# Optimization experiments

Measured on AMD Instinct MI355X. Metric: run time of the kernel, lower is better.

## Reference

```python
import jax, jax.numpy as jnp
import numpy as np

N_NODES = 100000
N_EDGES = 1250000
IN_DIM, HID_DIM, OUT_DIM = 128, 64, 64
NUM_LAYERS = 3
EPS = 1e-12  # F.normalize eps


def setup_inputs() -> dict:
    key = jax.random.key(0)
    ks = jax.random.split(key, 10)
    s = 0.05
    x = jax.random.normal(ks[0], (N_NODES, IN_DIM), dtype=jnp.float32)
    edge_index = jax.random.randint(ks[1], (2, N_EDGES), 0, N_NODES, dtype=jnp.int32)
    W1 = jax.random.normal(ks[2], (IN_DIM, HID_DIM), dtype=jnp.float32) * s
    b1 = jax.random.normal(ks[3], (HID_DIM,), dtype=jnp.float32) * s
    Wl = jax.random.normal(ks[4], (NUM_LAYERS, HID_DIM, HID_DIM), dtype=jnp.float32) * s
    bl = jax.random.normal(ks[5], (NUM_LAYERS, HID_DIM), dtype=jnp.float32) * s
    Wr = jax.random.normal(ks[6], (NUM_LAYERS, HID_DIM, HID_DIM), dtype=jnp.float32) * s
    W2 = jax.random.normal(ks[7], (HID_DIM, OUT_DIM), dtype=jnp.float32) * s
    b2 = jax.random.normal(ks[8], (OUT_DIM,), dtype=jnp.float32) * s
    return {"x": x, "edge_index": edge_index, "W1": W1, "b1": b1,
            "Wl": Wl, "bl": bl, "Wr": Wr, "W2": W2, "b2": b2}


def reference(x, edge_index, W1, b1, Wl, bl, Wr, W2, b2):
    n = x.shape[0]
    src, dst = edge_index[0], edge_index[1]
    # in-degree for mean aggregation (zero-degree -> aggregate stays 0)
    deg = jax.ops.segment_sum(jnp.ones_like(dst, dtype=x.dtype), dst, num_segments=n)
    inv_deg = jnp.where(deg > 0, 1.0 / jnp.maximum(deg, 1.0), 0.0)[:, None]  # [n,1]
    h = x @ W1 + b1  # [n, hid]
    for i in range(Wl.shape[0]):
        # gather source features, scatter-mean to destinations
        agg = jax.ops.segment_sum(h[src], dst, num_segments=n) * inv_deg  # [n, hid]
        o = agg @ Wl[i] + bl[i] + h @ Wr[i]
        # row-wise L2 normalize (PyG normalize=True)
        norm = jnp.sqrt(jnp.sum(o * o, axis=-1, keepdims=True))
        o = o / jnp.maximum(norm, EPS)
        h = jax.nn.relu(o)
    return h @ W2 + b2
```

## Files before the change

### kernel.cpp

```cpp
#include <hip/hip_runtime.h>
#include <hip/hip_bf16.h>


#define NT 256
#define BATCH 4096
#define SBCAP 8192
#define HSTRIDE 72

typedef __attribute__((ext_vector_type(8))) short bf16x8;
typedef __attribute__((ext_vector_type(4))) float f32x4;

__device__ __forceinline__ float bfbits2f(unsigned short b) {
    return __uint_as_float(((unsigned)b) << 16);
}
__device__ __forceinline__ unsigned short f2bfbits(float v) {
    __hip_bfloat16 b = __float2bfloat16(v);
    return *reinterpret_cast<unsigned short*>(&b);
}


__global__ __launch_bounds__(NT) void bin1_kernel(const int* __restrict__ src,
    const int* __restrict__ dst, int m, unsigned* __restrict__ gcur,
    unsigned* __restrict__ bins) {
    __shared__ unsigned hist[256];
    __shared__ unsigned gbase[256];
    const int t = threadIdx.x;
    const int base = blockIdx.x * BATCH;
    hist[t] = 0;
    __syncthreads();
    int d[16], s[16];
    const int e0 = base + t * 16;
    const bool full = (base + BATCH) <= m;
    if (full) {
        #pragma unroll
        for (int q = 0; q < 4; ++q) {
            const int4 dv = *(const int4*)&dst[e0 + q * 4];
            const int4 sv = *(const int4*)&src[e0 + q * 4];
            d[q*4+0]=dv.x; d[q*4+1]=dv.y; d[q*4+2]=dv.z; d[q*4+3]=dv.w;
            s[q*4+0]=sv.x; s[q*4+1]=sv.y; s[q*4+2]=sv.z; s[q*4+3]=sv.w;
        }
        #pragma unroll
        for (int q = 0; q < 16; ++q) atomicAdd(&hist[d[q] >> 9], 1u);
    } else {
        #pragma unroll
        for (int q = 0; q < 16; ++q) {
            const int e = e0 + q;
            if (e < m) { d[q] = dst[e]; s[q] = src[e]; atomicAdd(&hist[d[q] >> 9], 1u); }
            else d[q] = -1;
        }
    }
    __syncthreads();
    {
        const unsigned h = hist[t];
        gbase[t] = h ? atomicAdd(&gcur[t], h) : 0u;
        hist[t] = 0;
    }
    __syncthreads();
    if (full) {
        #pragma unroll
        for (int q = 0; q < 16; ++q) {
            const int b = d[q] >> 9;
            const unsigned slot = gbase[b] + atomicAdd(&hist[b], 1u);
            bins[(size_t)b * SBCAP + slot] = ((unsigned)s[q] << 9) | (unsigned)(d[q] & 511);
        }
    } else {
        #pragma unroll
        for (int q = 0; q < 16; ++q) {
            if (d[q] >= 0) {
                const int b = d[q] >> 9;
                const unsigned slot = gbase[b] + atomicAdd(&hist[b], 1u);
                bins[(size_t)b * SBCAP + slot] = ((unsigned)s[q] << 9) | (unsigned)(d[q] & 511);
            }
        }
    }
}

__global__ __launch_bounds__(NT) void bin2_kernel(const unsigned* __restrict__ bins,
    const unsigned* __restrict__ gcur, int* __restrict__ row_ptr, int* __restrict__ csr,
    int n, int nsb, int m) {
    __shared__ unsigned hist[512];
    __shared__ unsigned off[512];
    __shared__ unsigned cur[512];
    __shared__ unsigned wsum[4];
    __shared__ unsigned gpre[256];
    const int k = blockIdx.x;
    const int t = threadIdx.x;
    const int lane = t & 63, wid = t >> 6;

    {
        const unsigned gv = (t < nsb) ? gcur[t] : 0u;
        unsigned gx = gv;
        #pragma unroll
        for (int o = 1; o < 64; o <<= 1) {
            const unsigned tt = __shfl_up(gx, o, 64);
            if (lane >= o) gx += tt;
        }
        if (lane == 63) wsum[wid] = gx;
        __syncthreads();
        unsigned wo = 0;
        for (int w = 0; w < wid; ++w) wo += wsum[w];
        gpre[t] = wo + gx - gv;
        __syncthreads();
    }
    const int cnt = (int)gcur[k];
    const unsigned sb = gpre[k];
    if (k == 0 && t == 0) row_ptr[n] = m;

    const unsigned* reg = bins + (size_t)k * SBCAP;
    hist[2*t] = 0; hist[2*t+1] = 0;
    __syncthreads();
    for (int i = t; i < cnt; i += NT) atomicAdd(&hist[reg[i] & 511u], 1u);
    __syncthreads();
    const unsigned v0 = hist[2*t], v1 = hist[2*t+1];
    const unsigned ps = v0 + v1;
    unsigned x = ps;
    #pragma unroll
    for (int o = 1; o < 64; o <<= 1) {
        const unsigned tt = __shfl_up(x, o, 64);
        if (lane >= o) x += tt;
    }
    if (lane == 63) wsum[wid] = x;
    __syncthreads();
    unsigned woff = 0;
    for (int w = 0; w < wid; ++w) woff += wsum[w];
    const unsigned excl = woff + x - ps;
    off[2*t] = excl; off[2*t+1] = excl + v0;
    cur[2*t] = 0; cur[2*t+1] = 0;
    const int node = k * 512 + 2 * t;
    if (node < n)     row_ptr[node]     = (int)(sb + excl);
    if (node + 1 < n) row_ptr[node + 1] = (int)(sb + excl + v0);
    __syncthreads();
    for (int i = t; i < cnt; i += NT) {
        const unsigned u = reg[i];
        const unsigned l = u & 511u;
        const unsigned r = atomicAdd(&cur[l], 1u);
        csr[sb + off[l] + r] = (int)(u >> 9);
    }
}


__global__ void wconv_kernel(const float* __restrict__ W1, const float* __restrict__ Wl,
                             const float* __restrict__ Wr, const float* __restrict__ W2,
                             unsigned short* __restrict__ out) {
    int i = blockIdx.x * blockDim.x + threadIdx.x;
    if (i >= 36864) return;
    float v;
    if (i < 8192) {
        const int col = i >> 7, k = i & 127;
        v = W1[k * 64 + col];
    } else if (i < 32768) {
        const int j = i - 8192;
        const int mm = j >> 13, r = j & 8191;
        const int isR = (r >> 12) & 1, q = r & 4095;
        const int col = q >> 6, k = q & 63;
        v = (isR ? Wr : Wl)[mm * 4096 + k * 64 + col];
    } else {
        const int q = i - 32768;
        const int col = q >> 6, k = q & 63;
        v = W2[k * 64 + col];
    }
    out[i] = f2bfbits(v);
}


__global__ __launch_bounds__(NT) void agg_kernel(const unsigned short* __restrict__ h,
    const int* __restrict__ row_ptr, const int* __restrict__ csr,
    unsigned short* __restrict__ aggB, int n) {
    const int t = threadIdx.x;
    const int lane = t & 63;
    const int g = lane >> 4;
    const int c = lane & 15;
    const int gw = (blockIdx.x * NT + t) >> 6;
    const int nw = (gridDim.x * NT) >> 6;
    for (int node = gw; node < n; node += nw) {
        const int rs = row_ptr[node];
        const int re = row_ptr[node + 1];
        float a0 = 0.f, a1 = 0.f, a2 = 0.f, a3 = 0.f;
        int e = rs;
        for (; e + 16 <= re; e += 16) {
            const int s0 = csr[e + g];
            const int s1 = csr[e + 4 + g];
            const int s2 = csr[e + 8 + g];
            const int s3 = csr[e + 12 + g];
            const ushort4 v0 = *(const ushort4*)&h[(size_t)s0 * 64 + c * 4];
            const ushort4 v1 = *(const ushort4*)&h[(size_t)s1 * 64 + c * 4];
            const ushort4 v2 = *(const ushort4*)&h[(size_t)s2 * 64 + c * 4];
            const ushort4 v3 = *(const ushort4*)&h[(size_t)s3 * 64 + c * 4];
            a0 += (bfbits2f(v0.x) + bfbits2f(v1.x)) + (bfbits2f(v2.x) + bfbits2f(v3.x));
            a1 += (bfbits2f(v0.y) + bfbits2f(v1.y)) + (bfbits2f(v2.y) + bfbits2f(v3.y));
            a2 += (bfbits2f(v0.z) + bfbits2f(v1.z)) + (bfbits2f(v2.z) + bfbits2f(v3.z));
            a3 += (bfbits2f(v0.w) + bfbits2f(v1.w)) + (bfbits2f(v2.w) + bfbits2f(v3.w));
        }
        for (; e + 8 <= re; e += 8) {
            const int s0 = csr[e + g];
            const int s1 = csr[e + 4 + g];
            const ushort4 v0 = *(const ushort4*)&h[(size_t)s0 * 64 + c * 4];
            const ushort4 v1 = *(const ushort4*)&h[(size_t)s1 * 64 + c * 4];
            a0 += bfbits2f(v0.x) + bfbits2f(v1.x);
            a1 += bfbits2f(v0.y) + bfbits2f(v1.y);
            a2 += bfbits2f(v0.z) + bfbits2f(v1.z);
            a3 += bfbits2f(v0.w) + bfbits2f(v1.w);
        }
        for (; e + 4 <= re; e += 4) {
            const int s0 = csr[e + g];
            const ushort4 v0 = *(const ushort4*)&h[(size_t)s0 * 64 + c * 4];
            a0 += bfbits2f(v0.x);
            a1 += bfbits2f(v0.y);
            a2 += bfbits2f(v0.z);
            a3 += bfbits2f(v0.w);
        }
        const int r = re - e;
        if (g < r) {
            const int s0 = csr[e + g];
            const ushort4 v0 = *(const ushort4*)&h[(size_t)s0 * 64 + c * 4];
            a0 += bfbits2f(v0.x);
            a1 += bfbits2f(v0.y);
            a2 += bfbits2f(v0.z);
            a3 += bfbits2f(v0.w);
        }
        a0 += __shfl_xor(a0, 16, 64); a0 += __shfl_xor(a0, 32, 64);
        a1 += __shfl_xor(a1, 16, 64); a1 += __shfl_xor(a1, 32, 64);
        a2 += __shfl_xor(a2, 16, 64); a2 += __shfl_xor(a2, 32, 64);
        a3 += __shfl_xor(a3, 16, 64); a3 += __shfl_xor(a3, 32, 64);
        if (g == 0) {
            const float inv = (re > rs) ? (1.0f / (float)(re - rs)) : 0.0f;
            ushort4 o;
            o.x = f2bfbits(a0 * inv);
            o.y = f2bfbits(a1 * inv);
            o.z = f2bfbits(a2 * inv);
            o.w = f2bfbits(a3 * inv);
            *(ushort4*)&aggB[(size_t)node * 64 + c * 4] = o;
        }
    }
}


template<int A1F32, int LAST>
__global__ __launch_bounds__(NT) void gemm_mfma(
    const float* __restrict__ A1f, const unsigned short* __restrict__ A1b,
    int ldA1, int K1, const unsigned short* __restrict__ W1t,
    const unsigned short* __restrict__ A2b, const unsigned short* __restrict__ W2t,
    const float* __restrict__ bias, float* __restrict__ outF,
    unsigned short* __restrict__ outB, int n, int do_norm,
    const unsigned short* __restrict__ W2t2, const float* __restrict__ b2) {
    const int t = threadIdx.x;
    const int lane = t & 63;
    const int w = t >> 6;
    const int r16 = lane & 15;
    const int g = lane >> 4;
    const int row0 = blockIdx.x * 128 + w * 32;

    f32x4 acc[2][4];
    #pragma unroll
    for (int i = 0; i < 2; ++i)
        #pragma unroll
        for (int j = 0; j < 4; ++j) {
            acc[i][j][0] = 0.f; acc[i][j][1] = 0.f; acc[i][j][2] = 0.f; acc[i][j][3] = 0.f;
        }

    int ra[2];
    #pragma unroll
    for (int rt = 0; rt < 2; ++rt) {
        int r = row0 + rt * 16 + r16;
        ra[rt] = (r < n) ? r : (n - 1);
    }

    #pragma unroll 1
    for (int kc = 0; kc < K1; kc += 32) {
        bf16x8 af[2];
        #pragma unroll
        for (int rt = 0; rt < 2; ++rt) {
            if (A1F32) {
                const float* p = &A1f[(size_t)ra[rt] * ldA1 + kc + g * 8];
                const float4 f0 = *(const float4*)p;
                const float4 f1 = *(const float4*)(p + 4);
                bf16x8 a;
                a[0] = (short)f2bfbits(f0.x); a[1] = (short)f2bfbits(f0.y);
                a[2] = (short)f2bfbits(f0.z); a[3] = (short)f2bfbits(f0.w);
                a[4] = (short)f2bfbits(f1.x); a[5] = (short)f2bfbits(f1.y);
                a[6] = (short)f2bfbits(f1.z); a[7] = (short)f2bfbits(f1.w);
                af[rt] = a;
            } else {
                af[rt] = *(const bf16x8*)&A1b[(size_t)ra[rt] * ldA1 + kc + g * 8];
            }
        }
        #pragma unroll
        for (int ct = 0; ct < 4; ++ct) {
            const bf16x8 bw = *(const bf16x8*)&W1t[(size_t)(ct * 16 + r16) * K1 + kc + g * 8];
            acc[0][ct] = __builtin_amdgcn_mfma_f32_16x16x32_bf16(af[0], bw, acc[0][ct], 0, 0, 0);
            acc[1][ct] = __builtin_amdgcn_mfma_f32_16x16x32_bf16(af[1], bw, acc[1][ct], 0, 0, 0);
        }
    }
    if (A2b) {
        #pragma unroll 1
        for (int kc = 0; kc < 64; kc += 32) {
            bf16x8 af[2];
            #pragma unroll
            for (int rt = 0; rt < 2; ++rt)
                af[rt] = *(const bf16x8*)&A2b[(size_t)ra[rt] * 64 + kc + g * 8];
            #pragma unroll
            for (int ct = 0; ct < 4; ++ct) {
                const bf16x8 bw = *(const bf16x8*)&W2t[(size_t)(ct * 16 + r16) * 64 + kc + g * 8];
                acc[0][ct] = __builtin_amdgcn_mfma_f32_16x16x32_bf16(af[0], bw, acc[0][ct], 0, 0, 0);
                acc[1][ct] = __builtin_amdgcn_mfma_f32_16x16x32_bf16(af[1], bw, acc[1][ct], 0, 0, 0);
            }
        }
    }

    float bcol[4];
    #pragma unroll
    for (int ct = 0; ct < 4; ++ct) bcol[ct] = bias[ct * 16 + r16];

    #pragma unroll
    for (int rt = 0; rt < 2; ++rt) {
        #pragma unroll
        for (int ct = 0; ct < 4; ++ct)
            #pragma unroll
            for (int reg = 0; reg < 4; ++reg) acc[rt][ct][reg] += bcol[ct];

        if (do_norm) {
            #pragma unroll
            for (int reg = 0; reg < 4; ++reg) {
                float ss = 0.f;
                #pragma unroll
                for (int ct = 0; ct < 4; ++ct) ss += acc[rt][ct][reg] * acc[rt][ct][reg];
                ss += __shfl_xor(ss, 1, 64);
                ss += __shfl_xor(ss, 2, 64);
                ss += __shfl_xor(ss, 4, 64);
                ss += __shfl_xor(ss, 8, 64);
                const float inv = 1.0f / fmaxf(sqrtf(ss), 1e-12f);
                #pragma unroll
                for (int ct = 0; ct < 4; ++ct)
                    acc[rt][ct][reg] = fmaxf(acc[rt][ct][reg] * inv, 0.0f);
            }
        }
    }

    if constexpr (!LAST) {
        #pragma unroll
        for (int rt = 0; rt < 2; ++rt) {
            const int rbase = row0 + rt * 16 + g * 4;
            #pragma unroll
            for (int reg = 0; reg < 4; ++reg) {
                const int rr = rbase + reg;
                if (rr < n) {
                    if (outB) {
                        #pragma unroll
                        for (int ct = 0; ct < 4; ++ct)
                            outB[(size_t)rr * 64 + ct * 16 + r16] = f2bfbits(acc[rt][ct][reg]);
                    } else {
                        #pragma unroll
                        for (int ct = 0; ct < 4; ++ct)
                            outF[(size_t)rr * 64 + ct * 16 + r16] = acc[rt][ct][reg];
                    }
                }
            }
        }
    } else {
        __shared__ unsigned short h3S[128][HSTRIDE];
        #pragma unroll
        for (int rt = 0; rt < 2; ++rt) {
            #pragma unroll
            for (int reg = 0; reg < 4; ++reg) {
                const int lr = w * 32 + rt * 16 + g * 4 + reg;
                #pragma unroll
                for (int ct = 0; ct < 4; ++ct)
                    h3S[lr][ct * 16 + r16] = f2bfbits(acc[rt][ct][reg]);
            }
        }
        __syncthreads();
        f32x4 acc2[2][4];
        #pragma unroll
        for (int i = 0; i < 2; ++i)
            #pragma unroll
            for (int j = 0; j < 4; ++j) { acc2[i][j][0]=0.f; acc2[i][j][1]=0.f; acc2[i][j][2]=0.f; acc2[i][j][3]=0.f; }
        #pragma unroll
        for (int kc = 0; kc < 64; kc += 32) {
            bf16x8 af[2];
            #pragma unroll
            for (int rt = 0; rt < 2; ++rt)
                af[rt] = *(const bf16x8*)&h3S[w * 32 + rt * 16 + r16][kc + g * 8];
            #pragma unroll
            for (int ct = 0; ct < 4; ++ct) {
                const bf16x8 bw = *(const bf16x8*)&W2t2[(size_t)(ct * 16 + r16) * 64 + kc + g * 8];
                acc2[0][ct] = __builtin_amdgcn_mfma_f32_16x16x32_bf16(af[0], bw, acc2[0][ct], 0, 0, 0);
                acc2[1][ct] = __builtin_amdgcn_mfma_f32_16x16x32_bf16(af[1], bw, acc2[1][ct], 0, 0, 0);
            }
        }
        float b2c[4];
        #pragma unroll
        for (int ct = 0; ct < 4; ++ct) b2c[ct] = b2[ct * 16 + r16];
        #pragma unroll
        for (int rt = 0; rt < 2; ++rt) {
            const int rbase = row0 + rt * 16 + g * 4;
            #pragma unroll
            for (int reg = 0; reg < 4; ++reg) {
                const int rr = rbase + reg;
                if (rr < n) {
                    #pragma unroll
                    for (int ct = 0; ct < 4; ++ct)
                        outF[(size_t)rr * 64 + ct * 16 + r16] = acc2[rt][ct][reg] + b2c[ct];
                }
            }
        }
    }
}


extern "C" void kernel_launch(void* const* d_in, const int* in_sizes, int n_in,
                              void* d_out, int out_size, void* d_ws, size_t ws_size,
                              hipStream_t stream) {
    const float* x  = (const float*)d_in[0];
    const int*   ei = (const int*)  d_in[1];
    const float* W1 = (const float*)d_in[2];
    const float* b1 = (const float*)d_in[3];
    const float* Wl = (const float*)d_in[4];
    const float* bl = (const float*)d_in[5];
    const float* Wr = (const float*)d_in[6];
    const float* W2 = (const float*)d_in[7];
    const float* b2 = (const float*)d_in[8];
    float* out = (float*)d_out;

    const int n = in_sizes[0] / 128;
    const int m = in_sizes[1] / 2;
    const int* src = ei;
    const int* dst = ei + m;

    const int nsb = (n + 511) >> 9;

    char* ws = (char*)d_ws;
    size_t off = 0;
    auto alloc = [&](size_t bytes) -> void* {
        void* p = ws + off;
        off = (off + bytes + 255) & ~(size_t)255;
        return p;
    };
    unsigned short* aggB    = (unsigned short*)alloc((size_t)n * 64 * 2);
    unsigned short* hbf     = (unsigned short*)alloc((size_t)n * 64 * 2);
    int*            row_ptr = (int*)alloc((size_t)(n + 1) * sizeof(int));
    unsigned*       gcur    = (unsigned*)alloc((size_t)nsb * 4);
    unsigned*       bins    = (unsigned*)alloc((size_t)nsb * SBCAP * 4);
    int*            csr     = (int*)alloc((size_t)m * 4);
    unsigned short* wt      = (unsigned short*)alloc(36864 * 2);

    const unsigned short* W1t = wt;
    const unsigned short* W2t = wt + 32768;

    hipMemsetAsync(gcur, 0, (size_t)nsb * 4, stream);

    const int nb1 = (m + BATCH - 1) / BATCH;
    const int gtiles = (n + 127) / 128;

    wconv_kernel<<<144, NT, 0, stream>>>(W1, Wl, Wr, W2, wt);

    gemm_mfma<1, 0><<<gtiles, NT, 0, stream>>>(x, nullptr, 128, 128, W1t,
                                               nullptr, nullptr, b1, nullptr, hbf, n, 0,
                                               nullptr, nullptr);

    bin1_kernel<<<nb1, NT, 0, stream>>>(src, dst, m, gcur, bins);
    bin2_kernel<<<nsb, NT, 0, stream>>>(bins, gcur, row_ptr, csr, n, nsb, m);

    for (int i = 0; i < 2; ++i) {
        agg_kernel<<<2048, NT, 0, stream>>>(hbf, row_ptr, csr, aggB, n);
        const unsigned short* Wlt = wt + 8192 + (size_t)i * 8192;
        const unsigned short* Wrt = Wlt + 4096;
        gemm_mfma<0, 0><<<gtiles, NT, 0, stream>>>(nullptr, aggB, 64, 64, Wlt,
                                                   hbf, Wrt, bl + (size_t)i * 64,
                                                   nullptr, hbf, n, 1, nullptr, nullptr);
    }
    agg_kernel<<<2048, NT, 0, stream>>>(hbf, row_ptr, csr, aggB, n);
    gemm_mfma<0, 1><<<gtiles, NT, 0, stream>>>(nullptr, aggB, 64, 64, wt + 8192 + 16384,
                                               hbf, wt + 8192 + 16384 + 4096, bl + 128,
                                               out, nullptr, n, 1, W2t, b2);
}
```

Measured before the change: 217.5 us.

## Split node features into four 16-column planes so gather working set fits cache

Hidden features are stored as four separate column planes of 16 bf16 each (n×16 per plane) instead of row-major n×64. Aggregation blocks are assigned to one plane each, so each wave gathers 32-byte slices and the per-plane working set (~3.2MB) is more likely to stay resident in L2/LLC during the random gather. The GEMM loads and stores are changed to match the planar layout. The cost is smaller gather transactions with more per-edge index loads, and the float output path of the GEMM is removed.

```diff
diff --git a/kernel.cpp b/kernel.cpp
--- a/kernel.cpp
+++ b/kernel.cpp
@@ -168,68 +168,48 @@
     unsigned short* __restrict__ aggB, int n) {
     const int t = threadIdx.x;
     const int lane = t & 63;
-    const int g = lane >> 4;
-    const int c = lane & 15;
-    const int gw = (blockIdx.x * NT + t) >> 6;
-    const int nw = (gridDim.x * NT) >> 6;
+    const int gs = lane >> 3;
+    const int c = lane & 7;
+    const int grp = blockIdx.x & 3;
+    const int gw = ((blockIdx.x >> 2) * NT + t) >> 6;
+    const int nw = ((gridDim.x >> 2) * NT) >> 6;
+    const unsigned short* hg = h + (size_t)grp * n * 16;
+    unsigned short* ag = aggB + (size_t)grp * n * 16;
     for (int node = gw; node < n; node += nw) {
         const int rs = row_ptr[node];
         const int re = row_ptr[node + 1];
-        float a0 = 0.f, a1 = 0.f, a2 = 0.f, a3 = 0.f;
+        float a0 = 0.f, a1 = 0.f;
         int e = rs;
         for (; e + 16 <= re; e += 16) {
-            const int s0 = csr[e + g];
-            const int s1 = csr[e + 4 + g];
-            const int s2 = csr[e + 8 + g];
-            const int s3 = csr[e + 12 + g];
-            const ushort4 v0 = *(const ushort4*)&h[(size_t)s0 * 64 + c * 4];
-            const ushort4 v1 = *(const ushort4*)&h[(size_t)s1 * 64 + c * 4];
-            const ushort4 v2 = *(const ushort4*)&h[(size_t)s2 * 64 + c * 4];
-            const ushort4 v3 = *(const ushort4*)&h[(size_t)s3 * 64 + c * 4];
-            a0 += (bfbits2f(v0.x) + bfbits2f(v1.x)) + (bfbits2f(v2.x) + bfbits2f(v3.x));
-            a1 += (bfbits2f(v0.y) + bfbits2f(v1.y)) + (bfbits2f(v2.y) + bfbits2f(v3.y));
-            a2 += (bfbits2f(v0.z) + bfbits2f(v1.z)) + (bfbits2f(v2.z) + bfbits2f(v3.z));
-            a3 += (bfbits2f(v0.w) + bfbits2f(v1.w)) + (bfbits2f(v2.w) + bfbits2f(v3.w));
-        }
-        for (; e + 8 <= re; e += 8) {
-            const int s0 = csr[e + g];
-            const int s1 = csr[e + 4 + g];
-            const ushort4 v0 = *(const ushort4*)&h[(size_t)s0 * 64 + c * 4];
-            const ushort4 v1 = *(const ushort4*)&h[(size_t)s1 * 64 + c * 4];
+            const int s0 = csr[e + gs];
+            const int s1 = csr[e + 8 + gs];
+            const ushort2 v0 = *(const ushort2*)&hg[(size_t)s0 * 16 + c * 2];
+            const ushort2 v1 = *(const ushort2*)&hg[(size_t)s1 * 16 + c * 2];
             a0 += bfbits2f(v0.x) + bfbits2f(v1.x);
             a1 += bfbits2f(v0.y) + bfbits2f(v1.y);
-            a2 += bfbits2f(v0.z) + bfbits2f(v1.z);
-            a3 += bfbits2f(v0.w) + bfbits2f(v1.w);
-        }
-        for (; e + 4 <= re; e += 4) {
-            const int s0 = csr[e + g];
-            const ushort4 v0 = *(const ushort4*)&h[(size_t)s0 * 64 + c * 4];
+        }
+        for (; e + 8 <= re; e += 8) {
+            const int s0 = csr[e + gs];
+            const ushort2 v0 = *(const ushort2*)&hg[(size_t)s0 * 16 + c * 2];
             a0 += bfbits2f(v0.x);
             a1 += bfbits2f(v0.y);
-            a2 += bfbits2f(v0.z);
-            a3 += bfbits2f(v0.w);
         }
         const int r = re - e;
-        if (g < r) {
-            const int s0 = csr[e + g];
-            const ushort4 v0 = *(const ushort4*)&h[(size_t)s0 * 64 + c * 4];
+        if (gs < r) {
+            const int s0 = csr[e + gs];
+            const ushort2 v0 = *(const ushort2*)&hg[(size_t)s0 * 16 + c * 2];
             a0 += bfbits2f(v0.x);
             a1 += bfbits2f(v0.y);
-            a2 += bfbits2f(v0.z);
-            a3 += bfbits2f(v0.w);
-        }
-        a0 += __shfl_xor(a0, 16, 64); a0 += __shfl_xor(a0, 32, 64);
-        a1 += __shfl_xor(a1, 16, 64); a1 += __shfl_xor(a1, 32, 64);
-        a2 += __shfl_xor(a2, 16, 64); a2 += __shfl_xor(a2, 32, 64);
-        a3 += __shfl_xor(a3, 16, 64); a3 += __shfl_xor(a3, 32, 64);
-        if (g == 0) {
+        }
+        a0 += __shfl_xor(a0, 8, 64);  a1 += __shfl_xor(a1, 8, 64);
+        a0 += __shfl_xor(a0, 16, 64); a1 += __shfl_xor(a1, 16, 64);
+        a0 += __shfl_xor(a0, 32, 64); a1 += __shfl_xor(a1, 32, 64);
+        if (gs == 0) {
             const float inv = (re > rs) ? (1.0f / (float)(re - rs)) : 0.0f;
-            ushort4 o;
+            ushort2 o;
             o.x = f2bfbits(a0 * inv);
             o.y = f2bfbits(a1 * inv);
-            o.z = f2bfbits(a2 * inv);
-            o.w = f2bfbits(a3 * inv);
-            *(ushort4*)&aggB[(size_t)node * 64 + c * 4] = o;
+            *(ushort2*)&ag[(size_t)node * 16 + c * 2] = o;
         }
     }
 }
@@ -281,7 +261,9 @@
                 a[6] = (short)f2bfbits(f1.z); a[7] = (short)f2bfbits(f1.w);
                 af[rt] = a;
             } else {
-                af[rt] = *(const bf16x8*)&A1b[(size_t)ra[rt] * ldA1 + kc + g * 8];
+                const int grp = (kc >> 4) + (g >> 1);
+                const int lo = (g & 1) * 8;
+                af[rt] = *(const bf16x8*)&A1b[((size_t)grp * n + ra[rt]) * 16 + lo];
             }
         }
         #pragma unroll
@@ -296,8 +278,11 @@
         for (int kc = 0; kc < 64; kc += 32) {
             bf16x8 af[2];
             #pragma unroll
-            for (int rt = 0; rt < 2; ++rt)
-                af[rt] = *(const bf16x8*)&A2b[(size_t)ra[rt] * 64 + kc + g * 8];
+            for (int rt = 0; rt < 2; ++rt) {
+                const int grp = (kc >> 4) + (g >> 1);
+                const int lo = (g & 1) * 8;
+                af[rt] = *(const bf16x8*)&A2b[((size_t)grp * n + ra[rt]) * 16 + lo];
+            }
             #pragma unroll
             for (int ct = 0; ct < 4; ++ct) {
                 const bf16x8 bw = *(const bf16x8*)&W2t[(size_t)(ct * 16 + r16) * 64 + kc + g * 8];
@@ -344,15 +329,9 @@
             for (int reg = 0; reg < 4; ++reg) {
                 const int rr = rbase + reg;
                 if (rr < n) {
-                    if (outB) {
-                        #pragma unroll
-                        for (int ct = 0; ct < 4; ++ct)
-                            outB[(size_t)rr * 64 + ct * 16 + r16] = f2bfbits(acc[rt][ct][reg]);
-                    } else {
-                        #pragma unroll
-                        for (int ct = 0; ct < 4; ++ct)
-                            outF[(size_t)rr * 64 + ct * 16 + r16] = acc[rt][ct][reg];
-                    }
+                    #pragma unroll
+                    for (int ct = 0; ct < 4; ++ct)
+                        outB[((size_t)ct * n + rr) * 16 + r16] = f2bfbits(acc[rt][ct][reg]);
                 }
             }
         }
```

Measured after the change: 345.1 us. 58.6% more time.

## Process two nodes per wavefront in aggregation and fold memset into wconv

Applied to the files above, without the earlier changes.

The aggregation kernel now splits each 64-lane wavefront into two halves, each handling a separate destination node with 2 edge groups instead of 4, and halves the shuffle reduction. With average degree around 12.5, this is meant to cut lane idling in the tail loops and the per-node reduction overhead. The separate memset of the bin counters is also replaced by zeroing inside the weight-conversion kernel, removing one launch. The memset fold relies on wconv's 36864 threads covering nsb, and on wconv running before bin1 on the same stream.

```diff
diff --git a/kernel.cpp b/kernel.cpp
--- a/kernel.cpp
+++ b/kernel.cpp
@@ -141,8 +141,10 @@
 
 __global__ void wconv_kernel(const float* __restrict__ W1, const float* __restrict__ Wl,
                              const float* __restrict__ Wr, const float* __restrict__ W2,
-                             unsigned short* __restrict__ out) {
+                             unsigned short* __restrict__ out, unsigned* __restrict__ gcur,
+                             int nsb) {
     int i = blockIdx.x * blockDim.x + threadIdx.x;
+    if (i < nsb) gcur[i] = 0u;
     if (i >= 36864) return;
     float v;
     if (i < 8192) {
@@ -168,20 +170,25 @@
     unsigned short* __restrict__ aggB, int n) {
     const int t = threadIdx.x;
     const int lane = t & 63;
-    const int g = lane >> 4;
+    const int half = lane >> 5;
+    const int gs = (lane >> 4) & 1;
     const int c = lane & 15;
     const int gw = (blockIdx.x * NT + t) >> 6;
     const int nw = (gridDim.x * NT) >> 6;
-    for (int node = gw; node < n; node += nw) {
-        const int rs = row_ptr[node];
-        const int re = row_ptr[node + 1];
+    const int npairs = (n + 1) >> 1;
+    for (int p = gw; p < npairs; p += nw) {
+        const int node = p * 2 + half;
+        const bool valid = node < n;
+        const int node_c = valid ? node : (n - 1);
+        const int rs = row_ptr[node_c];
+        const int re = row_ptr[node_c + 1];
         float a0 = 0.f, a1 = 0.f, a2 = 0.f, a3 = 0.f;
         int e = rs;
-        for (; e + 16 <= re; e += 16) {
-            const int s0 = csr[e + g];
-            const int s1 = csr[e + 4 + g];
-            const int s2 = csr[e + 8 + g];
-            const int s3 = csr[e + 12 + g];
+        for (; e + 8 <= re; e += 8) {
+            const int s0 = csr[e + gs];
+            const int s1 = csr[e + 2 + gs];
+            const int s2 = csr[e + 4 + gs];
+            const int s3 = csr[e + 6 + gs];
             const ushort4 v0 = *(const ushort4*)&h[(size_t)s0 * 64 + c * 4];
             const ushort4 v1 = *(const ushort4*)&h[(size_t)s1 * 64 + c * 4];
             const ushort4 v2 = *(const ushort4*)&h[(size_t)s2 * 64 + c * 4];
@@ -191,9 +198,9 @@
             a2 += (bfbits2f(v0.z) + bfbits2f(v1.z)) + (bfbits2f(v2.z) + bfbits2f(v3.z));
             a3 += (bfbits2f(v0.w) + bfbits2f(v1.w)) + (bfbits2f(v2.w) + bfbits2f(v3.w));
         }
-        for (; e + 8 <= re; e += 8) {
-            const int s0 = csr[e + g];
-            const int s1 = csr[e + 4 + g];
+        for (; e + 4 <= re; e += 4) {
+            const int s0 = csr[e + gs];
+            const int s1 = csr[e + 2 + gs];
             const ushort4 v0 = *(const ushort4*)&h[(size_t)s0 * 64 + c * 4];
             const ushort4 v1 = *(const ushort4*)&h[(size_t)s1 * 64 + c * 4];
             a0 += bfbits2f(v0.x) + bfbits2f(v1.x);
@@ -201,28 +208,27 @@
             a2 += bfbits2f(v0.z) + bfbits2f(v1.z);
             a3 += bfbits2f(v0.w) + bfbits2f(v1.w);
         }
-        for (; e + 4 <= re; e += 4) {
-            const int s0 = csr[e + g];
+        for (; e + 2 <= re; e += 2) {
+            const int s0 = csr[e + gs];
             const ushort4 v0 = *(const ushort4*)&h[(size_t)s0 * 64 + c * 4];
             a0 += bfbits2f(v0.x);
             a1 += bfbits2f(v0.y);
             a2 += bfbits2f(v0.z);
             a3 += bfbits2f(v0.w);
         }
-        const int r = re - e;
-        if (g < r) {
-            const int s0 = csr[e + g];
+        if (gs < re - e) {
+            const int s0 = csr[e + gs];
             const ushort4 v0 = *(const ushort4*)&h[(size_t)s0 * 64 + c * 4];
             a0 += bfbits2f(v0.x);
             a1 += bfbits2f(v0.y);
             a2 += bfbits2f(v0.z);
             a3 += bfbits2f(v0.w);
         }
-        a0 += __shfl_xor(a0, 16, 64); a0 += __shfl_xor(a0, 32, 64);
-        a1 += __shfl_xor(a1, 16, 64); a1 += __shfl_xor(a1, 32, 64);
-        a2 += __shfl_xor(a2, 16, 64); a2 += __shfl_xor(a2, 32, 64);
-        a3 += __shfl_xor(a3, 16, 64); a3 += __shfl_xor(a3, 32, 64);
-        if (g == 0) {
+        a0 += __shfl_xor(a0, 16, 64);
+        a1 += __shfl_xor(a1, 16, 64);
+        a2 += __shfl_xor(a2, 16, 64);
+        a3 += __shfl_xor(a3, 16, 64);
+        if (gs == 0 && valid) {
             const float inv = (re > rs) ? (1.0f / (float)(re - rs)) : 0.0f;
             ushort4 o;
             o.x = f2bfbits(a0 * inv);
@@ -446,12 +452,10 @@
     const unsigned short* W1t = wt;
     const unsigned short* W2t = wt + 32768;
 
-    hipMemsetAsync(gcur, 0, (size_t)nsb * 4, stream);
-
     const int nb1 = (m + BATCH - 1) / BATCH;
     const int gtiles = (n + 127) / 128;
 
-    wconv_kernel<<<144, NT, 0, stream>>>(W1, Wl, Wr, W2, wt);
+    wconv_kernel<<<144, NT, 0, stream>>>(W1, Wl, Wr, W2, wt, gcur, nsb);
 
     gemm_mfma<1, 0><<<gtiles, NT, 0, stream>>>(x, nullptr, 128, 128, W1t,
                                                nullptr, nullptr, b1, nullptr, hbf, n, 0,
```

Result: faster. 204.4 us (-6.0%).
